# Performance work log

Hardware: AMD Instinct MI355X
Metric: run time of the kernel (lower is better)

The kernel has to match this reference:

```python
import jax, jax.numpy as jnp
import numpy as np

B, N, R = 16, 512, 10
DE, DR, DOUT = 256, 64, 256

def setup_inputs() -> dict:
    key = jax.random.key(0)
    k1, k2, k3, k4 = jax.random.split(key, 4)
    node_features = jax.random.normal(k1, (B, N, DE), dtype=jnp.float32)
    relation_features = jax.random.normal(k2, (B, R, DR), dtype=jnp.float32)
    adj = jax.random.uniform(k3, (B, R, N, N), dtype=jnp.float32)
    in_dim = (DE + DR) * R
    bound = float(np.sqrt(6.0 / (in_dim + DOUT)))  # xavier_uniform
    W = jax.random.uniform(k4, (DOUT, in_dim), dtype=jnp.float32, minval=-bound, maxval=bound)
    bias = jnp.zeros((DOUT,), dtype=jnp.float32)
    return {"node_features": node_features, "relation_features": relation_features,
            "adj": adj, "W": W, "bias": bias}

def reference(node_features, relation_features, adj, W, bias):
    # adj: [B,R,N,N]; node_features: [B,N,De]; relation_features: [B,R,Dr]
    # Per relation r: bmm(adj[:,r], cat([node, rel_r broadcast], -1))
    # Node part: adj @ node_features for every relation at once.
    node_part = jnp.einsum('brnm,bmd->brnd', adj, node_features)      # [B,R,N,De]
    # Relation part: adj @ (rel_r repeated over rows) == rowsum(adj) * rel_r
    rel_part = adj.sum(axis=-1)[..., None] * relation_features[:, :, None, :]  # [B,R,N,Dr]
    supports = jnp.concatenate([node_part, rel_part], axis=-1)        # [B,R,N,De+Dr]
    supports = supports.transpose(0, 2, 1, 3).reshape(node_features.shape[0],
                                                      node_features.shape[1], -1)  # [B,N,R*(De+Dr)]
    return supports @ W.T + bias
```

## Files before the change

kernel.cpp:

```cpp
#include <hip/hip_runtime.h>
#include <stdint.h>

#define B_     16
#define N_     512
#define R_     10
#define DE_    256
#define DR_    64
#define DOUT_  256
#define INDIM_ 3200
#define BLK_   320
#define RN_    5120

typedef __bf16          v8bf  __attribute__((ext_vector_type(8)));
typedef unsigned short  v8us  __attribute__((ext_vector_type(8)));
typedef float           f32x4 __attribute__((ext_vector_type(4)));

static __device__ __forceinline__ unsigned short f2b(float f) {
  union { float f; unsigned u; } c; c.f = f;
  unsigned r = c.u + 0x7FFFu + ((c.u >> 16) & 1u);
  return (unsigned short)(r >> 16);
}

static __device__ __forceinline__ v8bf us2bf(v8us u) {
  union { v8us u; v8bf b; } c; c.u = u; return c.b;
}

static __device__ __forceinline__ void gl_lds16(const void* g, void* l) {
  __builtin_amdgcn_global_load_lds(
      (const __attribute__((address_space(1))) void*)g,
      (__attribute__((address_space(3))) void*)l, 16, 0, 0);
}

__global__ void conv_adj(const float* __restrict__ adj, unsigned short* __restrict__ adjB) {
  const size_t base = (size_t)blockIdx.x * 8192;
  const int tid = threadIdx.x;
#pragma unroll
  for (int p = 0; p < 4; ++p) {
    size_t off = base + (size_t)p * 2048 + (size_t)tid * 8;
    float4 x = *(const float4*)(adj + off);
    float4 y = *(const float4*)(adj + off + 4);
    v8us u;
    u[0] = f2b(x.x); u[1] = f2b(x.y); u[2] = f2b(x.z); u[3] = f2b(x.w);
    u[4] = f2b(y.x); u[5] = f2b(y.y); u[6] = f2b(y.z); u[7] = f2b(y.w);
    *(v8us*)(adjB + off) = u;
  }
}

__global__ void prep_nodeB(const float* __restrict__ nf, unsigned short* __restrict__ nodeB) {
  const size_t base = (size_t)blockIdx.x * 8192;
  const int tid = threadIdx.x;
#pragma unroll
  for (int p = 0; p < 4; ++p) {
    size_t off = base + (size_t)p * 2048 + (size_t)tid * 8;
    float4 x = *(const float4*)(nf + off);
    float4 y = *(const float4*)(nf + off + 4);
    v8us u;
    u[0] = f2b(x.x); u[1] = f2b(x.y); u[2] = f2b(x.z); u[3] = f2b(x.w);
    u[4] = f2b(y.x); u[5] = f2b(y.y); u[6] = f2b(y.z); u[7] = f2b(y.w);
    *(v8us*)(nodeB + off) = u;
  }
}

__global__ void prep_W(const float* __restrict__ W, unsigned short* __restrict__ Wn) {
  int idx = blockIdx.x * 256 + threadIdx.x;
  int r = idx >> 16;
  int o = (idx >> 8) & 255;
  int d = idx & 255;
  Wn[idx] = f2b(W[(size_t)o * INDIM_ + r * BLK_ + d]);
}

__global__ void prep_U(const float* __restrict__ rel, const float* __restrict__ W,
                       float* __restrict__ Uf) {
  int idx = blockIdx.x * 256 + threadIdx.x;
  int o  = idx & 255;
  int br = idx >> 8;
  int r  = br % R_;
  const float* rp = rel + (size_t)br * DR_;
  const float* wp = W + (size_t)o * INDIM_ + r * BLK_ + DE_;
  float v = 0.f;
#pragma unroll 8
  for (int d = 0; d < DR_; ++d) v += rp[d] * wp[d];
  Uf[idx] = v;
}

__global__ void out_init(const float* __restrict__ bias, float* __restrict__ out) {
  int idx = blockIdx.x * 256 + threadIdx.x;
  float4 bv = *(const float4*)(bias + (idx & 63) * 4);
  *(float4*)(out + (size_t)idx * 4) = bv;
}

__global__ void stageA_gemm(const unsigned short* __restrict__ nodeB,
                            const unsigned short* __restrict__ WnB,
                            const float* __restrict__ Uf,
                            unsigned short* __restrict__ Gp) {
  __shared__ unsigned short Al[128 * 64];
  __shared__ unsigned short Bl[128 * 64];
  const int br = blockIdx.x;
  const int b  = br / R_, r = br % R_;
  const int o0 = blockIdx.y * 128;
  const int m0 = blockIdx.z * 128;
  const int tid  = threadIdx.x;
  const int lane = tid & 63;
  const int wave = tid >> 6;
  const int wm = wave >> 1, wn = wave & 1;
  const int quad = lane >> 4, l16 = lane & 15;

  const unsigned short* Wb = WnB + (size_t)r * (DOUT_ * DE_);
  const unsigned short* Nb = nodeB + (size_t)b * (N_ * DE_);

  f32x4 acc[4][4];
#pragma unroll
  for (int i = 0; i < 4; ++i)
#pragma unroll
    for (int j = 0; j < 4; ++j) acc[i][j] = f32x4{0.f, 0.f, 0.f, 0.f};

  for (int dk = 0; dk < DE_; dk += 64) {
#pragma unroll
    for (int it = 0; it < 4; ++it) {
      int rowblk = it * 32 + wave * 8;
      int rl = rowblk + (lane >> 3);
      int kc = (lane & 7) ^ (rl & 7);
      gl_lds16(Wb + (size_t)(o0 + rl) * DE_ + dk + kc * 8, Al + rowblk * 64);
      gl_lds16(Nb + (size_t)(m0 + rl) * DE_ + dk + kc * 8, Bl + rowblk * 64);
    }
    __syncthreads();
#pragma unroll
    for (int ks = 0; ks < 2; ++ks) {
      const int kb = ks * 4;
      v8bf av[4], bv[4];
#pragma unroll
      for (int mi = 0; mi < 4; ++mi) {
        int m = wm * 64 + mi * 16 + l16;
        av[mi] = us2bf(*(const v8us*)(Al + m * 64 + (((kb + quad) ^ (m & 7)) * 8)));
      }
#pragma unroll
      for (int ni = 0; ni < 4; ++ni) {
        int c = wn * 64 + ni * 16 + l16;
        bv[ni] = us2bf(*(const v8us*)(Bl + c * 64 + (((kb + quad) ^ (c & 7)) * 8)));
      }
#pragma unroll
      for (int mi = 0; mi < 4; ++mi)
#pragma unroll
        for (int ni = 0; ni < 4; ++ni)
          acc[mi][ni] = __builtin_amdgcn_mfma_f32_16x16x32_bf16(av[mi], bv[ni], acc[mi][ni], 0, 0, 0);
    }
    __syncthreads();
  }

#pragma unroll
  for (int mi = 0; mi < 4; ++mi)
#pragma unroll
    for (int t = 0; t < 4; ++t) {
      int o = o0 + wm * 64 + mi * 16 + quad * 4 + t;
      float u = Uf[(size_t)br * DOUT_ + o];
      unsigned short* grow = Gp + ((size_t)(b * DOUT_ + o)) * RN_ + r * N_ + m0;
#pragma unroll
      for (int ni = 0; ni < 4; ++ni) {
        int m = wn * 64 + ni * 16 + l16;
        grow[m] = f2b(acc[mi][ni][t] + u);
      }
    }
}

__global__ void stageB_gemm(const unsigned short* __restrict__ adjB,
                            const unsigned short* __restrict__ Gp,
                            float* __restrict__ out) {
  __shared__ unsigned short Al[128 * 64];
  __shared__ unsigned short Bl[128 * 64];
  const int b  = blockIdx.x;
  const int n0 = blockIdx.y * 128;
  const int o0 = (blockIdx.z & 1) * 128;
  const int sp = blockIdx.z >> 1;
  const int tid  = threadIdx.x;
  const int lane = tid & 63;
  const int wave = tid >> 6;
  const int wm = wave >> 1, wn = wave & 1;
  const int quad = lane >> 4, l16 = lane & 15;

  const unsigned short* Ab = adjB + (size_t)b * (R_ * N_ * N_);
  const unsigned short* Gb = Gp + (size_t)b * (DOUT_ * RN_);

  f32x4 acc[4][4];
#pragma unroll
  for (int i = 0; i < 4; ++i)
#pragma unroll
    for (int j = 0; j < 4; ++j) acc[i][j] = f32x4{0.f, 0.f, 0.f, 0.f};

  for (int it = 0; it < 20; ++it) {
    const int k0 = sp * 1280 + it * 64;
    const int r  = k0 >> 9;
    const int mo = k0 & 511;
#pragma unroll
    for (int s = 0; s < 4; ++s) {
      int rowblk = s * 32 + wave * 8;
      int rl = rowblk + (lane >> 3);
      int kc = (lane & 7) ^ (rl & 7);
      gl_lds16(Ab + (size_t)r * (N_ * N_) + (size_t)(n0 + rl) * N_ + mo + kc * 8,
               Al + rowblk * 64);
      gl_lds16(Gb + (size_t)(o0 + rl) * RN_ + k0 + kc * 8, Bl + rowblk * 64);
    }
    __syncthreads();
#pragma unroll
    for (int ks = 0; ks < 2; ++ks) {
      const int kb = ks * 4;
      v8bf av[4], bv[4];
#pragma unroll
      for (int mi = 0; mi < 4; ++mi) {
        int m = wm * 64 + mi * 16 + l16;
        av[mi] = us2bf(*(const v8us*)(Al + m * 64 + (((kb + quad) ^ (m & 7)) * 8)));
      }
#pragma unroll
      for (int ni = 0; ni < 4; ++ni) {
        int c = wn * 64 + ni * 16 + l16;
        bv[ni] = us2bf(*(const v8us*)(Bl + c * 64 + (((kb + quad) ^ (c & 7)) * 8)));
      }
#pragma unroll
      for (int mi = 0; mi < 4; ++mi)
#pragma unroll
        for (int ni = 0; ni < 4; ++ni)
          acc[mi][ni] = __builtin_amdgcn_mfma_f32_16x16x32_bf16(av[mi], bv[ni], acc[mi][ni], 0, 0, 0);
    }
    __syncthreads();
  }

  float* outb = out + (size_t)b * (N_ * DOUT_);
#pragma unroll
  for (int mi = 0; mi < 4; ++mi)
#pragma unroll
    for (int t = 0; t < 4; ++t) {
      int row = n0 + wm * 64 + mi * 16 + quad * 4 + t;
#pragma unroll
      for (int ni = 0; ni < 4; ++ni) {
        int col = o0 + wn * 64 + ni * 16 + l16;
        atomicAdd(outb + (size_t)row * DOUT_ + col, acc[mi][ni][t]);
      }
    }
}

extern "C" void kernel_launch(void* const* d_in, const int* in_sizes, int n_in,
                              void* d_out, int out_size, void* d_ws, size_t ws_size,
                              hipStream_t stream) {
  const float* node = (const float*)d_in[0];
  const float* rel  = (const float*)d_in[1];
  const float* adj  = (const float*)d_in[2];
  const float* W    = (const float*)d_in[3];
  const float* bias = (const float*)d_in[4];
  float* out = (float*)d_out;

  char* ws = (char*)d_ws;
  unsigned short* adjB  = (unsigned short*)(ws);
  unsigned short* nodeB = (unsigned short*)(ws + ((size_t)88  << 20));
  unsigned short* WnB   = (unsigned short*)(ws + ((size_t)93  << 20));
  float*          Uf    = (float*)         (ws + ((size_t)95  << 20));
  unsigned short* Gp    = (unsigned short*)(ws + ((size_t)96  << 20));

  conv_adj<<<dim3((B_ * R_ * N_ * N_) / 8192), 256, 0, stream>>>(adj, adjB);
  prep_nodeB<<<dim3((B_ * N_ * DE_) / 8192), 256, 0, stream>>>(node, nodeB);
  prep_W<<<dim3((R_ * DOUT_ * DE_) / 256), 256, 0, stream>>>(W, WnB);
  prep_U<<<dim3((B_ * R_ * DOUT_) / 256), 256, 0, stream>>>(rel, W, Uf);
  stageA_gemm<<<dim3(B_ * R_, DOUT_ / 128, N_ / 128), 256, 0, stream>>>(nodeB, WnB, Uf, Gp);
  out_init<<<dim3((B_ * N_ * DOUT_ / 4) / 256), 256, 0, stream>>>(bias, out);
  stageB_gemm<<<dim3(B_, N_ / 128, 2 * 4), 256, 0, stream>>>(adjB, Gp, out);
}
```

Before: 354.5 us.

## Fuse fp32-to-bf16 adjacency conversion into stage-B GEMM with register prefetch

Removes the separate conv_adj pass that wrote a bf16 copy of the 168 MB fp32 adjacency tensor. The stage-B GEMM now reads fp32 adj directly, prefetches the next tile into registers, converts it to bf16 and stores it swizzled into LDS. The tiling also changes: each block covers 64 rows by the full 256 outputs with a 5-way K split over relation pairs. This trades a full write and re-read of a bf16 adj copy for fp32 global reads inside the GEMM, with more register pressure and conversion work on the critical path.

```diff
diff --git a/kernel.cpp b/kernel.cpp
--- a/kernel.cpp
+++ b/kernel.cpp
@@ -29,21 +29,6 @@
   __builtin_amdgcn_global_load_lds(
       (const __attribute__((address_space(1))) void*)g,
       (__attribute__((address_space(3))) void*)l, 16, 0, 0);
-}
-
-__global__ void conv_adj(const float* __restrict__ adj, unsigned short* __restrict__ adjB) {
-  const size_t base = (size_t)blockIdx.x * 8192;
-  const int tid = threadIdx.x;
-#pragma unroll
-  for (int p = 0; p < 4; ++p) {
-    size_t off = base + (size_t)p * 2048 + (size_t)tid * 8;
-    float4 x = *(const float4*)(adj + off);
-    float4 y = *(const float4*)(adj + off + 4);
-    v8us u;
-    u[0] = f2b(x.x); u[1] = f2b(x.y); u[2] = f2b(x.z); u[3] = f2b(x.w);
-    u[4] = f2b(y.x); u[5] = f2b(y.y); u[6] = f2b(y.z); u[7] = f2b(y.w);
-    *(v8us*)(adjB + off) = u;
-  }
 }
 
 __global__ void prep_nodeB(const float* __restrict__ nf, unsigned short* __restrict__ nodeB) {
@@ -162,22 +147,21 @@
     }
 }
 
-__global__ void stageB_gemm(const unsigned short* __restrict__ adjB,
-                            const unsigned short* __restrict__ Gp,
-                            float* __restrict__ out) {
-  __shared__ unsigned short Al[128 * 64];
-  __shared__ unsigned short Bl[128 * 64];
+__global__ __launch_bounds__(256, 3)
+void stageB_gemm(const float* __restrict__ adj,
+                 const unsigned short* __restrict__ Gp,
+                 float* __restrict__ out) {
+  __shared__ unsigned short Al[64 * 64];
+  __shared__ unsigned short Bl[256 * 64];
   const int b  = blockIdx.x;
-  const int n0 = blockIdx.y * 128;
-  const int o0 = (blockIdx.z & 1) * 128;
-  const int sp = blockIdx.z >> 1;
+  const int n0 = blockIdx.y * 64;
+  const int sp = blockIdx.z;
   const int tid  = threadIdx.x;
   const int lane = tid & 63;
   const int wave = tid >> 6;
-  const int wm = wave >> 1, wn = wave & 1;
   const int quad = lane >> 4, l16 = lane & 15;
 
-  const unsigned short* Ab = adjB + (size_t)b * (R_ * N_ * N_);
+  const float* Ab = adj + (size_t)b * (R_ * N_ * N_);
   const unsigned short* Gb = Gp + (size_t)b * (DOUT_ * RN_);
 
   f32x4 acc[4][4];
@@ -186,18 +170,47 @@
 #pragma unroll
     for (int j = 0; j < 4; ++j) acc[i][j] = f32x4{0.f, 0.f, 0.f, 0.f};
 
-  for (int it = 0; it < 20; ++it) {
-    const int k0 = sp * 1280 + it * 64;
-    const int r  = k0 >> 9;
-    const int mo = k0 & 511;
-#pragma unroll
-    for (int s = 0; s < 4; ++s) {
+  const int arow = tid >> 2;
+  const int acb  = tid & 3;
+  const float* arp = Ab + (size_t)(n0 + arow) * N_ + acb * 16;
+
+  float4 p0, p1, p2, p3;
+  {
+    const float* g = arp + (size_t)(sp * 2) * (N_ * N_);
+    p0 = *(const float4*)(g);
+    p1 = *(const float4*)(g + 4);
+    p2 = *(const float4*)(g + 8);
+    p3 = *(const float4*)(g + 12);
+  }
+
+  for (int it = 0; it < 16; ++it) {
+    const int r  = sp * 2 + (it >> 3);
+    const int k0 = r * N_ + (it & 7) * 64;
+#pragma unroll
+    for (int s = 0; s < 8; ++s) {
       int rowblk = s * 32 + wave * 8;
       int rl = rowblk + (lane >> 3);
       int kc = (lane & 7) ^ (rl & 7);
-      gl_lds16(Ab + (size_t)r * (N_ * N_) + (size_t)(n0 + rl) * N_ + mo + kc * 8,
-               Al + rowblk * 64);
-      gl_lds16(Gb + (size_t)(o0 + rl) * RN_ + k0 + kc * 8, Bl + rowblk * 64);
+      gl_lds16(Gb + (size_t)rl * RN_ + k0 + kc * 8, Bl + rowblk * 64);
+    }
+    {
+      v8us u0, u1;
+      u0[0] = f2b(p0.x); u0[1] = f2b(p0.y); u0[2] = f2b(p0.z); u0[3] = f2b(p0.w);
+      u0[4] = f2b(p1.x); u0[5] = f2b(p1.y); u0[6] = f2b(p1.z); u0[7] = f2b(p1.w);
+      u1[0] = f2b(p2.x); u1[1] = f2b(p2.y); u1[2] = f2b(p2.z); u1[3] = f2b(p2.w);
+      u1[4] = f2b(p3.x); u1[5] = f2b(p3.y); u1[6] = f2b(p3.z); u1[7] = f2b(p3.w);
+      int c0 = (acb * 2)     ^ (arow & 7);
+      int c1 = (acb * 2 + 1) ^ (arow & 7);
+      *(v8us*)(Al + arow * 64 + c0 * 8) = u0;
+      *(v8us*)(Al + arow * 64 + c1 * 8) = u1;
+    }
+    if (it < 15) {
+      const int rn = sp * 2 + ((it + 1) >> 3);
+      const float* g = arp + (size_t)rn * (N_ * N_) + ((it + 1) & 7) * 64;
+      p0 = *(const float4*)(g);
+      p1 = *(const float4*)(g + 4);
+      p2 = *(const float4*)(g + 8);
+      p3 = *(const float4*)(g + 12);
     }
     __syncthreads();
 #pragma unroll
@@ -206,13 +219,13 @@
       v8bf av[4], bv[4];
 #pragma unroll
       for (int mi = 0; mi < 4; ++mi) {
-        int m = wm * 64 + mi * 16 + l16;
+        int m = mi * 16 + l16;
         av[mi] = us2bf(*(const v8us*)(Al + m * 64 + (((kb + quad) ^ (m & 7)) * 8)));
       }
 #pragma unroll
       for (int ni = 0; ni < 4; ++ni) {
-        int c = wn * 64 + ni * 16 + l16;
-        bv[ni] = us2bf(*(const v8us*)(Bl + c * 64 + (((kb + quad) ^ (c & 7)) * 8)));
+        int o = wave * 64 + ni * 16 + l16;
+        bv[ni] = us2bf(*(const v8us*)(Bl + o * 64 + (((kb + quad) ^ (o & 7)) * 8)));
       }
 #pragma unroll
       for (int mi = 0; mi < 4; ++mi)
@@ -228,10 +241,10 @@
   for (int mi = 0; mi < 4; ++mi)
 #pragma unroll
     for (int t = 0; t < 4; ++t) {
-      int row = n0 + wm * 64 + mi * 16 + quad * 4 + t;
-#pragma unroll
-      for (int ni = 0; ni < 4; ++ni) {
-        int col = o0 + wn * 64 + ni * 16 + l16;
+      int row = n0 + mi * 16 + quad * 4 + t;
+#pragma unroll
+      for (int ni = 0; ni < 4; ++ni) {
+        int col = wave * 64 + ni * 16 + l16;
         atomicAdd(outb + (size_t)row * DOUT_ + col, acc[mi][ni][t]);
       }
     }
@@ -248,17 +261,15 @@
   float* out = (float*)d_out;
 
   char* ws = (char*)d_ws;
-  unsigned short* adjB  = (unsigned short*)(ws);
-  unsigned short* nodeB = (unsigned short*)(ws + ((size_t)88  << 20));
-  unsigned short* WnB   = (unsigned short*)(ws + ((size_t)93  << 20));
-  float*          Uf    = (float*)         (ws + ((size_t)95  << 20));
-  unsigned short* Gp    = (unsigned short*)(ws + ((size_t)96  << 20));
-
-  conv_adj<<<dim3((B_ * R_ * N_ * N_) / 8192), 256, 0, stream>>>(adj, adjB);
+  unsigned short* nodeB = (unsigned short*)(ws);
+  unsigned short* WnB   = (unsigned short*)(ws + ((size_t)5 << 20));
+  float*          Uf    = (float*)         (ws + ((size_t)7 << 20));
+  unsigned short* Gp    = (unsigned short*)(ws + ((size_t)8 << 20));
+
   prep_nodeB<<<dim3((B_ * N_ * DE_) / 8192), 256, 0, stream>>>(node, nodeB);
   prep_W<<<dim3((R_ * DOUT_ * DE_) / 256), 256, 0, stream>>>(W, WnB);
   prep_U<<<dim3((B_ * R_ * DOUT_) / 256), 256, 0, stream>>>(rel, W, Uf);
   stageA_gemm<<<dim3(B_ * R_, DOUT_ / 128, N_ / 128), 256, 0, stream>>>(nodeB, WnB, Uf, Gp);
   out_init<<<dim3((B_ * N_ * DOUT_ / 4) / 256), 256, 0, stream>>>(bias, out);
-  stageB_gemm<<<dim3(B_, N_ / 128, 2 * 4), 256, 0, stream>>>(adjB, Gp, out);
-}
+  stageB_gemm<<<dim3(B_, N_ / 64, 5), 256, 0, stream>>>(adj, Gp, out);
+}
```

Result: faster. 321.0 us (-9.4%).
